# Kernel optimization log

Hardware: AMD Instinct MI355X
Metric: run time of the kernel (lower is better)

## Reference

```python
import jax, jax.numpy as jnp
import numpy as np

B, L, C, H = 4, 2048, 1024, 16
D = C // H            # head_dim = 64
HALF = D // 2         # 32
MAX_SCALE_MUL = float(np.log(100.0))


def setup_inputs() -> dict:
    key = jax.random.key(0)
    ks = jax.random.split(key, 6)
    x = jax.random.normal(ks[0], (B, L, C), dtype=jnp.float32)
    # causal additive bias [1,1,L,L]
    causal = jnp.tril(jnp.ones((L, L), dtype=bool))
    attn_bias = jnp.where(causal, 0.0, -1e9).astype(jnp.float32)[None, None]
    # RoPE cos/sin table: [B, 2, L, half]
    inv_freq = 1.0 / (10000.0 ** (jnp.arange(HALF, dtype=jnp.float32) / HALF))
    ang = jnp.arange(L, dtype=jnp.float32)[:, None] * inv_freq[None, :]  # [L, half]
    rope = jnp.stack([jnp.cos(ang), jnp.sin(ang)], axis=0)               # [2, L, half]
    rope_batch = jnp.broadcast_to(rope[None], (B, 2, L, HALF)).astype(jnp.float32)
    mat_qkv_w = jax.random.normal(ks[1], (3 * C, C), dtype=jnp.float32) * (1.0 / np.sqrt(C))
    q_bias = jnp.zeros((C,), dtype=jnp.float32)
    v_bias = jnp.zeros((C,), dtype=jnp.float32)
    proj_w = jax.random.normal(ks[2], (C, C), dtype=jnp.float32) * (1.0 / np.sqrt(C))
    proj_b = jnp.zeros((C,), dtype=jnp.float32)
    scale_mul = jnp.full((1, H, 1, 1), np.log(4.0), dtype=jnp.float32)
    return {"x": x, "attn_bias": attn_bias, "rope_batch": rope_batch,
            "mat_qkv_w": mat_qkv_w, "q_bias": q_bias, "v_bias": v_bias,
            "proj_w": proj_w, "proj_b": proj_b, "scale_mul": scale_mul}


def _l2norm(t, eps=1e-12):
    # F.normalize(t, dim=-1)
    n = jnp.sqrt(jnp.sum(t * t, axis=-1, keepdims=True))
    return t / jnp.maximum(n, eps)


def reference(x, attn_bias, rope_batch, mat_qkv_w, q_bias, v_bias, proj_w, proj_b, scale_mul):
    b, l, c = x.shape
    bias_cat = jnp.concatenate([q_bias, jnp.zeros_like(q_bias), v_bias])  # [3C]
    qkv = (x @ mat_qkv_w.T + bias_cat).reshape(b, l, 3, H, D)
    # non-flash layout: BHLc
    q = jnp.transpose(qkv[:, :, 0], (0, 2, 1, 3))
    k = jnp.transpose(qkv[:, :, 1], (0, 2, 1, 3))
    v = jnp.transpose(qkv[:, :, 2], (0, 2, 1, 3))
    # attn_l2_norm: scale=1, per-head learned multiplier
    sm = jnp.exp(jnp.minimum(scale_mul, MAX_SCALE_MUL))  # [1,H,1,1]
    q = _l2norm(q) * sm
    k = _l2norm(k)
    # RoPE (interleaved even/odd dims), start=0
    cos = rope_batch[:, 0, :l, :][:, None]  # [B,1,L,half]
    sin = rope_batch[:, 1, :l, :][:, None]
    def rot(t):
        t0, t1 = t[..., ::2], t[..., 1::2]
        r0 = t0 * cos - t1 * sin
        r1 = t0 * sin + t1 * cos
        return jnp.stack([r0, r1], axis=-1).reshape(t.shape)
    q, k = rot(q), rot(k)
    scale = 1.0  # attn_l2_norm path
    scores = jnp.einsum('bhqd,bhkd->bhqk', q, k) * scale + attn_bias
    attn = jax.nn.softmax(scores, axis=-1)
    out = jnp.einsum('bhqk,bhkd->bhqd', attn, v)
    out = jnp.transpose(out, (0, 2, 1, 3)).reshape(b, l, c)
    return out @ proj_w.T + proj_b
```

## Files before the change

### kernel.cpp

```cpp
#include <hip/hip_runtime.h>
#include <hip/hip_bf16.h>

#define BB 4
#define LL 2048
#define CC 1024
#define HH 16
#define DD 64
#define HALFD 32

typedef short bf16x8 __attribute__((ext_vector_type(8)));
typedef short bf16x4 __attribute__((ext_vector_type(4)));
typedef float f32x4 __attribute__((ext_vector_type(4)));

#if defined(__has_builtin)
#if __has_builtin(__builtin_amdgcn_mfma_f32_16x16x16bf16_1k)
#define HAVE_MFMA16 1
#endif
#endif

__device__ __forceinline__ float bf2f(unsigned short u) {
    union { unsigned int i; float f; } x; x.i = ((unsigned int)u) << 16; return x.f;
}
__device__ __forceinline__ unsigned short f2bf(float f) {
    union { float f; unsigned int i; } x; x.f = f;
    return (unsigned short)((x.i + 0x7fffu + ((x.i >> 16) & 1u)) >> 16);
}

__global__ void k_f2bf(const float4* __restrict__ in, ushort4* __restrict__ out, int n4) {
    int i = blockIdx.x * blockDim.x + threadIdx.x;
    if (i < n4) {
        float4 v = in[i];
        ushort4 o;
        o.x = f2bf(v.x); o.y = f2bf(v.y); o.z = f2bf(v.z); o.w = f2bf(v.w);
        out[i] = o;
    }
}

__global__ void k_biascat(const float* __restrict__ qb, const float* __restrict__ vb,
                          float* __restrict__ out) {
    int i = blockIdx.x * blockDim.x + threadIdx.x;
    if (i < 3 * CC) out[i] = (i < CC) ? qb[i] : (i < 2 * CC ? 0.f : vb[i - 2 * CC]);
}

template <typename OutT>
__global__ __launch_bounds__(256) void k_gemm_bt(
    const unsigned short* __restrict__ A, const unsigned short* __restrict__ Bt,
    const float* __restrict__ bias, OutT* __restrict__ Cout, int M, int N, int K) {
    __shared__ unsigned short As[128][40];
    __shared__ unsigned short Bs[128][40];
    int nT = N >> 7;
    int tM = (blockIdx.x / nT) << 7;
    int tN = (blockIdx.x % nT) << 7;
    int t = threadIdx.x;
    int lane = t & 63, wid = t >> 6;
    int wr = (wid >> 1) * 64, wc = (wid & 1) * 64;
    int c = lane & 15, g = lane >> 4;
    f32x4 acc[4][4];
#pragma unroll
    for (int i = 0; i < 4; i++)
#pragma unroll
        for (int j = 0; j < 4; j++) acc[i][j] = (f32x4){0.f, 0.f, 0.f, 0.f};

    for (int k0 = 0; k0 < K; k0 += 32) {
        __syncthreads();
#pragma unroll
        for (int i = t; i < 512; i += 256) {
            int row = i >> 2, ch = (i & 3) << 3;
            *(bf16x8*)&As[row][ch] = *(const bf16x8*)&A[(size_t)(tM + row) * K + k0 + ch];
            *(bf16x8*)&Bs[row][ch] = *(const bf16x8*)&Bt[(size_t)(tN + row) * K + k0 + ch];
        }
        __syncthreads();
        bf16x8 af[4], bfr[4];
#pragma unroll
        for (int fm = 0; fm < 4; fm++) af[fm] = *(const bf16x8*)&As[wr + fm * 16 + c][g * 8];
#pragma unroll
        for (int fn = 0; fn < 4; fn++) bfr[fn] = *(const bf16x8*)&Bs[wc + fn * 16 + c][g * 8];
#pragma unroll
        for (int fm = 0; fm < 4; fm++)
#pragma unroll
            for (int fn = 0; fn < 4; fn++)
                acc[fm][fn] = __builtin_amdgcn_mfma_f32_16x16x32_bf16(af[fm], bfr[fn],
                                                                      acc[fm][fn], 0, 0, 0);
    }
#pragma unroll
    for (int fm = 0; fm < 4; fm++) {
#pragma unroll
        for (int fn = 0; fn < 4; fn++) {
            int col = tN + wc + fn * 16 + c;
            float bv = bias[col];
#pragma unroll
            for (int r = 0; r < 4; r++) {
                int row = tM + wr + fm * 16 + g * 4 + r;
                float v = acc[fm][fn][r] + bv;
                if constexpr (sizeof(OutT) == 2)
                    Cout[(size_t)row * N + col] = f2bf(v);
                else
                    Cout[(size_t)row * N + col] = v;
            }
        }
    }
}

__global__ __launch_bounds__(256) void k_qknorm(
    const unsigned short* __restrict__ qkv, const float* __restrict__ rope,
    const float* __restrict__ smul, unsigned short* __restrict__ Q,
    unsigned short* __restrict__ Ko) {
    int wid = threadIdx.x >> 6, lane = threadIdx.x & 63;
    long rowid = (long)blockIdx.x * 4 + wid;
    int h = rowid & 15;
    long t2 = rowid >> 4;
    int l = t2 & 2047;
    int b = (int)(t2 >> 11);
    size_t base = ((size_t)(b * LL + l) * 3) * CC + h * 64 + lane;
    float q = bf2f(qkv[base]);
    float k = bf2f(qkv[base + CC]);
    float sq = q * q, sk = k * k;
#pragma unroll
    for (int m = 32; m >= 1; m >>= 1) {
        sq += __shfl_xor(sq, m);
        sk += __shfl_xor(sk, m);
    }
    float sm = expf(fminf(smul[h], 4.6051701859880913680f));
    q = q / fmaxf(sqrtf(sq), 1e-12f) * sm;
    k = k / fmaxf(sqrtf(sk), 1e-12f);
    int j = lane >> 1;
    float cs = rope[((size_t)(b * 2) * LL + l) * HALFD + j];
    float sn = rope[((size_t)(b * 2 + 1) * LL + l) * HALFD + j];
    float qp = __shfl_xor(q, 1), kp = __shfl_xor(k, 1);
    float qn = (lane & 1) ? (qp * sn + q * cs) : (q * cs - qp * sn);
    float kn = (lane & 1) ? (kp * sn + k * cs) : (k * cs - kp * sn);
    size_t ob = ((size_t)(b * HH + h) * LL + l) * 64 + lane;
    Q[ob] = f2bf(qn);
    Ko[ob] = f2bf(kn);
}

__global__ __launch_bounds__(256) void k_vtrans(const unsigned short* __restrict__ qkv,
                                               unsigned short* __restrict__ Vt) {
    __shared__ unsigned short tile[64][65];
    int bid = blockIdx.x;
    int lb = bid & 31;
    int bh = bid >> 5;
    int h = bh & 15, b = bh >> 4;
    int t = threadIdx.x;
    for (int i = t; i < 4096; i += 256) {
        int row = i >> 6, dd = i & 63;
        tile[row][dd] = qkv[((size_t)(b * LL + lb * 64 + row) * 3 + 2) * CC + h * 64 + dd];
    }
    __syncthreads();
    for (int i = t; i < 4096; i += 256) {
        int dd = i >> 6, l2 = i & 63;
        Vt[((size_t)bh * 64 + dd) * LL + lb * 64 + l2] = tile[l2][dd];
    }
}

__global__ __launch_bounds__(256) void k_attn(
    const unsigned short* __restrict__ Q, const unsigned short* __restrict__ K,
    const unsigned short* __restrict__ Vt, unsigned short* __restrict__ Out) {
    int lane = threadIdx.x & 63, wid = threadIdx.x >> 6;
    int c = lane & 15, g = lane >> 4;
    int bid = blockIdx.x;
    int bh = bid & 63;
    int strip = 15 - (bid >> 6);
    int qb = strip * 128 + wid * 32;
    const unsigned short* Qh = Q + (size_t)bh * LL * 64;
    const unsigned short* Kh = K + (size_t)bh * LL * 64;
    const unsigned short* Vh = Vt + (size_t)bh * 64 * LL;

    bf16x8 qf[2][2];
#pragma unroll
    for (int qt = 0; qt < 2; qt++)
#pragma unroll
        for (int ch = 0; ch < 2; ch++)
            qf[qt][ch] =
                *(const bf16x8*)&Qh[(size_t)(qb + qt * 16 + c) * 64 + ch * 32 + g * 8];

    f32x4 acc[2][4];
#pragma unroll
    for (int qt = 0; qt < 2; qt++)
#pragma unroll
        for (int dt = 0; dt < 4; dt++) acc[qt][dt] = (f32x4){0.f, 0.f, 0.f, 0.f};
    float m_[2] = {-1e30f, -1e30f}, l_[2] = {0.f, 0.f};

#ifndef HAVE_MFMA16
    int srcA = 32 * (g & 1) + c;
    int srcB = srcA + 16;
#endif

    for (int kt = 0; kt < qb + 32; kt += 32) {
        bf16x8 kf[2][2];
#pragma unroll
        for (int kt2 = 0; kt2 < 2; kt2++)
#pragma unroll
            for (int ch = 0; ch < 2; ch++)
                kf[kt2][ch] =
                    *(const bf16x8*)&Kh[(size_t)(kt + kt2 * 16 + c) * 64 + ch * 32 + g * 8];
#ifdef HAVE_MFMA16
        bf16x4 vf[4][2];
#pragma unroll
        for (int dt = 0; dt < 4; dt++)
#pragma unroll
            for (int kt2 = 0; kt2 < 2; kt2++)
                vf[dt][kt2] =
                    *(const bf16x4*)&Vh[(size_t)(dt * 16 + c) * LL + kt + kt2 * 16 + 4 * g];
#else
        bf16x8 vf8[4];
#pragma unroll
        for (int dt = 0; dt < 4; dt++)
            vf8[dt] = *(const bf16x8*)&Vh[(size_t)(dt * 16 + c) * LL + kt + 8 * g];
#endif
#pragma unroll
        for (int qt = 0; qt < 2; qt++) {
            int qtb = qb + qt * 16;
            int qrow = qtb + c;
            f32x4 s0 = (f32x4){0.f, 0.f, 0.f, 0.f}, s1 = (f32x4){0.f, 0.f, 0.f, 0.f};
            s0 = __builtin_amdgcn_mfma_f32_16x16x32_bf16(kf[0][0], qf[qt][0], s0, 0, 0, 0);
            s0 = __builtin_amdgcn_mfma_f32_16x16x32_bf16(kf[0][1], qf[qt][1], s0, 0, 0, 0);
            s1 = __builtin_amdgcn_mfma_f32_16x16x32_bf16(kf[1][0], qf[qt][0], s1, 0, 0, 0);
            s1 = __builtin_amdgcn_mfma_f32_16x16x32_bf16(kf[1][1], qf[qt][1], s1, 0, 0, 0);
            if (kt + 31 > qtb) {
#pragma unroll
                for (int r = 0; r < 4; r++) {
                    if (kt + 4 * g + r > qrow) s0[r] = -1e9f;
                    if (kt + 16 + 4 * g + r > qrow) s1[r] = -1e9f;
                }
            }
            float tm = fmaxf(fmaxf(fmaxf(s0[0], s0[1]), fmaxf(s0[2], s0[3])),
                             fmaxf(fmaxf(s1[0], s1[1]), fmaxf(s1[2], s1[3])));
            tm = fmaxf(tm, __shfl_xor(tm, 16));
            tm = fmaxf(tm, __shfl_xor(tm, 32));
            float mn = fmaxf(m_[qt], tm);
            float p0[4], p1[4];
            float rs = 0.f;
#pragma unroll
            for (int r = 0; r < 4; r++) {
                p0[r] = __expf(s0[r] - mn);
                p1[r] = __expf(s1[r] - mn);
                rs += p0[r] + p1[r];
            }
            rs += __shfl_xor(rs, 16);
            rs += __shfl_xor(rs, 32);
            float scl = __expf(m_[qt] - mn);
            l_[qt] = l_[qt] * scl + rs;
            m_[qt] = mn;
#pragma unroll
            for (int dt = 0; dt < 4; dt++) {
                acc[qt][dt][0] *= scl; acc[qt][dt][1] *= scl;
                acc[qt][dt][2] *= scl; acc[qt][dt][3] *= scl;
            }
#ifdef HAVE_MFMA16
            bf16x4 pb0, pb1;
#pragma unroll
            for (int r = 0; r < 4; r++) {
                pb0[r] = (short)f2bf(p0[r]);
                pb1[r] = (short)f2bf(p1[r]);
            }
#pragma unroll
            for (int dt = 0; dt < 4; dt++) {
                acc[qt][dt] =
                    __builtin_amdgcn_mfma_f32_16x16x16bf16_1k(vf[dt][0], pb0, acc[qt][dt], 0, 0, 0);
                acc[qt][dt] =
                    __builtin_amdgcn_mfma_f32_16x16x16bf16_1k(vf[dt][1], pb1, acc[qt][dt], 0, 0, 0);
            }
#else
            unsigned int A0 = (unsigned int)f2bf(p0[0]) | ((unsigned int)f2bf(p0[1]) << 16);
            unsigned int A1 = (unsigned int)f2bf(p0[2]) | ((unsigned int)f2bf(p0[3]) << 16);
            unsigned int B0 = (unsigned int)f2bf(p1[0]) | ((unsigned int)f2bf(p1[1]) << 16);
            unsigned int B1 = (unsigned int)f2bf(p1[2]) | ((unsigned int)f2bf(p1[3]) << 16);
            int t0a = __shfl((int)A0, srcA), t0b = __shfl((int)B0, srcA);
            int t1a = __shfl((int)A1, srcA), t1b = __shfl((int)B1, srcA);
            int t2a = __shfl((int)A0, srcB), t2b = __shfl((int)B0, srcB);
            int t3a = __shfl((int)A1, srcB), t3b = __shfl((int)B1, srcB);
            union { int w[4]; bf16x8 v; } u;
            bool hi = (g & 2) != 0;
            u.w[0] = hi ? t0b : t0a;
            u.w[1] = hi ? t1b : t1a;
            u.w[2] = hi ? t2b : t2a;
            u.w[3] = hi ? t3b : t3a;
#pragma unroll
            for (int dt = 0; dt < 4; dt++)
                acc[qt][dt] =
                    __builtin_amdgcn_mfma_f32_16x16x32_bf16(vf8[dt], u.v, acc[qt][dt], 0, 0, 0);
#endif
        }
    }
    int b = bh >> 4, h = bh & 15;
#pragma unroll
    for (int qt = 0; qt < 2; qt++) {
        float inv = 1.f / l_[qt];
        int qg = qb + qt * 16 + c;
        size_t ob = ((size_t)b * LL + qg) * CC + h * 64;
#pragma unroll
        for (int dt = 0; dt < 4; dt++) {
            ushort4 o;
            o.x = f2bf(acc[qt][dt][0] * inv);
            o.y = f2bf(acc[qt][dt][1] * inv);
            o.z = f2bf(acc[qt][dt][2] * inv);
            o.w = f2bf(acc[qt][dt][3] * inv);
            *(ushort4*)&Out[ob + dt * 16 + 4 * g] = o;
        }
    }
}

extern "C" void kernel_launch(void* const* d_in, const int* in_sizes, int n_in,
                              void* d_out, int out_size, void* d_ws, size_t ws_size,
                              hipStream_t stream) {
    const float* x = (const float*)d_in[0];
    const float* rope = (const float*)d_in[2];
    const float* w1 = (const float*)d_in[3];
    const float* qb = (const float*)d_in[4];
    const float* vb = (const float*)d_in[5];
    const float* w2 = (const float*)d_in[6];
    const float* pb = (const float*)d_in[7];
    const float* smul = (const float*)d_in[8];
    float* out = (float*)d_out;

    char* ws = (char*)d_ws;
    unsigned short* xb = (unsigned short*)(ws + 0);
    unsigned short* w1b = (unsigned short*)(ws + 16777216);
    unsigned short* w2b = (unsigned short*)(ws + 23068672);
    float* biascat = (float*)(ws + 25165824);
    unsigned short* qkvb = (unsigned short*)(ws + 25178112);
    unsigned short* Qb = (unsigned short*)(ws + 75509760);
    unsigned short* Kb = (unsigned short*)(ws + 92286976);
    unsigned short* Vtb = (unsigned short*)(ws + 109064192);
    unsigned short* attb = (unsigned short*)(ws + 125841408);
    if (ws_size < 142618624) return;

    int n4;
    n4 = BB * LL * CC / 4;
    k_f2bf<<<(n4 + 255) / 256, 256, 0, stream>>>((const float4*)x, (ushort4*)xb, n4);
    n4 = 3 * CC * CC / 4;
    k_f2bf<<<(n4 + 255) / 256, 256, 0, stream>>>((const float4*)w1, (ushort4*)w1b, n4);
    n4 = CC * CC / 4;
    k_f2bf<<<(n4 + 255) / 256, 256, 0, stream>>>((const float4*)w2, (ushort4*)w2b, n4);
    k_biascat<<<12, 256, 0, stream>>>(qb, vb, biascat);

    k_gemm_bt<unsigned short><<<(8192 / 128) * (3072 / 128), 256, 0, stream>>>(
        xb, w1b, biascat, qkvb, BB * LL, 3 * CC, CC);

    k_qknorm<<<BB * LL * HH / 4, 256, 0, stream>>>(qkvb, rope, smul, Qb, Kb);
    k_vtrans<<<BB * HH * (LL / 64), 256, 0, stream>>>(qkvb, Vtb);
    k_attn<<<64 * 16, 256, 0, stream>>>(Qb, Kb, Vtb, attb);

    k_gemm_bt<float><<<(8192 / 128) * (1024 / 128), 256, 0, stream>>>(
        attb, w2b, pb, out, BB * LL, CC, CC);
}
```

Baseline: 354.4 us.

## Use direct global-to-LDS loads in GEMM and widen attention key tiles with lazy rescale

The GEMM staging loop now uses global_load_lds to copy A/B tiles straight into unpadded shared memory, skipping the trip through registers. The attention loop processes 64 keys per iteration instead of 32, which halves the number of softmax reductions and loop iterations. It also skips the running-max rescale unless the max grows by more than a threshold of 8. Removing the padding may cause LDS bank conflicts on the fragment reads. The lazy rescale lets probabilities exceed 1 before bf16 conversion. With a 64-key step, the loop bound qb+32 can read keys past the diagonal, though those are masked.

```diff
diff --git a/kernel.cpp b/kernel.cpp
--- a/kernel.cpp
+++ b/kernel.cpp
@@ -24,6 +24,11 @@
 __device__ __forceinline__ unsigned short f2bf(float f) {
     union { float f; unsigned int i; } x; x.f = f;
     return (unsigned short)((x.i + 0x7fffu + ((x.i >> 16) & 1u)) >> 16);
+}
+__device__ __forceinline__ void gload_lds16(const void* g, void* l) {
+    __builtin_amdgcn_global_load_lds(
+        (const __attribute__((address_space(1))) unsigned int*)g,
+        (__attribute__((address_space(3))) unsigned int*)l, 16, 0, 0);
 }
 
 __global__ void k_f2bf(const float4* __restrict__ in, ushort4* __restrict__ out, int n4) {
@@ -46,8 +51,8 @@
 __global__ __launch_bounds__(256) void k_gemm_bt(
     const unsigned short* __restrict__ A, const unsigned short* __restrict__ Bt,
     const float* __restrict__ bias, OutT* __restrict__ Cout, int M, int N, int K) {
-    __shared__ unsigned short As[128][40];
-    __shared__ unsigned short Bs[128][40];
+    __shared__ unsigned short As[128][32];
+    __shared__ unsigned short Bs[128][32];
     int nT = N >> 7;
     int tM = (blockIdx.x / nT) << 7;
     int tN = (blockIdx.x % nT) << 7;
@@ -55,6 +60,15 @@
     int lane = t & 63, wid = t >> 6;
     int wr = (wid >> 1) * 64, wc = (wid & 1) * 64;
     int c = lane & 15, g = lane >> 4;
+
+    const unsigned short* gA = A + (size_t)(tM + wid * 32 + (lane >> 2)) * K + (lane & 3) * 8;
+    const unsigned short* gB = Bt + (size_t)(tN + wid * 32 + (lane >> 2)) * K + (lane & 3) * 8;
+    unsigned short* lA0 = &As[wid * 32][0];
+    unsigned short* lA1 = &As[wid * 32 + 16][0];
+    unsigned short* lB0 = &Bs[wid * 32][0];
+    unsigned short* lB1 = &Bs[wid * 32 + 16][0];
+    size_t r16 = (size_t)16 * K;
+
     f32x4 acc[4][4];
 #pragma unroll
     for (int i = 0; i < 4; i++)
@@ -63,12 +77,10 @@
 
     for (int k0 = 0; k0 < K; k0 += 32) {
         __syncthreads();
-#pragma unroll
-        for (int i = t; i < 512; i += 256) {
-            int row = i >> 2, ch = (i & 3) << 3;
-            *(bf16x8*)&As[row][ch] = *(const bf16x8*)&A[(size_t)(tM + row) * K + k0 + ch];
-            *(bf16x8*)&Bs[row][ch] = *(const bf16x8*)&Bt[(size_t)(tN + row) * K + k0 + ch];
-        }
+        gload_lds16(gA + k0, lA0);
+        gload_lds16(gA + k0 + r16, lA1);
+        gload_lds16(gB + k0, lB0);
+        gload_lds16(gB + k0 + r16, lB1);
         __syncthreads();
         bf16x8 af[4], bfr[4];
 #pragma unroll
@@ -186,100 +198,122 @@
     int srcB = srcA + 16;
 #endif
 
-    for (int kt = 0; kt < qb + 32; kt += 32) {
-        bf16x8 kf[2][2];
-#pragma unroll
-        for (int kt2 = 0; kt2 < 2; kt2++)
+    for (int kt = 0; kt < qb + 32; kt += 64) {
+        bf16x8 kf[4][2];
+#pragma unroll
+        for (int kt2 = 0; kt2 < 4; kt2++)
 #pragma unroll
             for (int ch = 0; ch < 2; ch++)
                 kf[kt2][ch] =
                     *(const bf16x8*)&Kh[(size_t)(kt + kt2 * 16 + c) * 64 + ch * 32 + g * 8];
 #ifdef HAVE_MFMA16
-        bf16x4 vf[4][2];
+        bf16x4 vf[4][4];
 #pragma unroll
         for (int dt = 0; dt < 4; dt++)
 #pragma unroll
-            for (int kt2 = 0; kt2 < 2; kt2++)
+            for (int kt2 = 0; kt2 < 4; kt2++)
                 vf[dt][kt2] =
                     *(const bf16x4*)&Vh[(size_t)(dt * 16 + c) * LL + kt + kt2 * 16 + 4 * g];
 #else
-        bf16x8 vf8[4];
+        bf16x8 vf8[4][2];
 #pragma unroll
         for (int dt = 0; dt < 4; dt++)
-            vf8[dt] = *(const bf16x8*)&Vh[(size_t)(dt * 16 + c) * LL + kt + 8 * g];
+#pragma unroll
+            for (int hf = 0; hf < 2; hf++)
+                vf8[dt][hf] =
+                    *(const bf16x8*)&Vh[(size_t)(dt * 16 + c) * LL + kt + hf * 32 + 8 * g];
 #endif
 #pragma unroll
         for (int qt = 0; qt < 2; qt++) {
             int qtb = qb + qt * 16;
             int qrow = qtb + c;
-            f32x4 s0 = (f32x4){0.f, 0.f, 0.f, 0.f}, s1 = (f32x4){0.f, 0.f, 0.f, 0.f};
-            s0 = __builtin_amdgcn_mfma_f32_16x16x32_bf16(kf[0][0], qf[qt][0], s0, 0, 0, 0);
-            s0 = __builtin_amdgcn_mfma_f32_16x16x32_bf16(kf[0][1], qf[qt][1], s0, 0, 0, 0);
-            s1 = __builtin_amdgcn_mfma_f32_16x16x32_bf16(kf[1][0], qf[qt][0], s1, 0, 0, 0);
-            s1 = __builtin_amdgcn_mfma_f32_16x16x32_bf16(kf[1][1], qf[qt][1], s1, 0, 0, 0);
-            if (kt + 31 > qtb) {
-#pragma unroll
-                for (int r = 0; r < 4; r++) {
-                    if (kt + 4 * g + r > qrow) s0[r] = -1e9f;
-                    if (kt + 16 + 4 * g + r > qrow) s1[r] = -1e9f;
+            f32x4 s[4];
+#pragma unroll
+            for (int kt2 = 0; kt2 < 4; kt2++) {
+                s[kt2] = (f32x4){0.f, 0.f, 0.f, 0.f};
+                s[kt2] = __builtin_amdgcn_mfma_f32_16x16x32_bf16(kf[kt2][0], qf[qt][0],
+                                                                 s[kt2], 0, 0, 0);
+                s[kt2] = __builtin_amdgcn_mfma_f32_16x16x32_bf16(kf[kt2][1], qf[qt][1],
+                                                                 s[kt2], 0, 0, 0);
+            }
+            if (kt + 63 > qtb) {
+#pragma unroll
+                for (int kt2 = 0; kt2 < 4; kt2++) {
+                    if (kt + kt2 * 16 + 15 > qtb) {
+#pragma unroll
+                        for (int r = 0; r < 4; r++)
+                            if (kt + kt2 * 16 + 4 * g + r > qrow) s[kt2][r] = -1e9f;
+                    }
                 }
             }
-            float tm = fmaxf(fmaxf(fmaxf(s0[0], s0[1]), fmaxf(s0[2], s0[3])),
-                             fmaxf(fmaxf(s1[0], s1[1]), fmaxf(s1[2], s1[3])));
+            float tm = fmaxf(fmaxf(fmaxf(s[0][0], s[0][1]), fmaxf(s[0][2], s[0][3])),
+                             fmaxf(fmaxf(s[1][0], s[1][1]), fmaxf(s[1][2], s[1][3])));
+            float tm2 = fmaxf(fmaxf(fmaxf(s[2][0], s[2][1]), fmaxf(s[2][2], s[2][3])),
+                              fmaxf(fmaxf(s[3][0], s[3][1]), fmaxf(s[3][2], s[3][3])));
+            tm = fmaxf(tm, tm2);
             tm = fmaxf(tm, __shfl_xor(tm, 16));
             tm = fmaxf(tm, __shfl_xor(tm, 32));
-            float mn = fmaxf(m_[qt], tm);
-            float p0[4], p1[4];
+            if (__any(tm > m_[qt] + 8.0f)) {
+                float mn = fmaxf(m_[qt], tm);
+                float scl = __expf(m_[qt] - mn);
+                m_[qt] = mn;
+                l_[qt] *= scl;
+#pragma unroll
+                for (int dt = 0; dt < 4; dt++) {
+                    acc[qt][dt][0] *= scl; acc[qt][dt][1] *= scl;
+                    acc[qt][dt][2] *= scl; acc[qt][dt][3] *= scl;
+                }
+            }
+            float p[4][4];
             float rs = 0.f;
 #pragma unroll
-            for (int r = 0; r < 4; r++) {
-                p0[r] = __expf(s0[r] - mn);
-                p1[r] = __expf(s1[r] - mn);
-                rs += p0[r] + p1[r];
-            }
+            for (int kt2 = 0; kt2 < 4; kt2++)
+#pragma unroll
+                for (int r = 0; r < 4; r++) {
+                    p[kt2][r] = __expf(s[kt2][r] - m_[qt]);
+                    rs += p[kt2][r];
+                }
             rs += __shfl_xor(rs, 16);
             rs += __shfl_xor(rs, 32);
-            float scl = __expf(m_[qt] - mn);
-            l_[qt] = l_[qt] * scl + rs;
-            m_[qt] = mn;
-#pragma unroll
-            for (int dt = 0; dt < 4; dt++) {
-                acc[qt][dt][0] *= scl; acc[qt][dt][1] *= scl;
-                acc[qt][dt][2] *= scl; acc[qt][dt][3] *= scl;
-            }
+            l_[qt] += rs;
 #ifdef HAVE_MFMA16
-            bf16x4 pb0, pb1;
-#pragma unroll
-            for (int r = 0; r < 4; r++) {
-                pb0[r] = (short)f2bf(p0[r]);
-                pb1[r] = (short)f2bf(p1[r]);
-            }
-#pragma unroll
-            for (int dt = 0; dt < 4; dt++) {
-                acc[qt][dt] =
-                    __builtin_amdgcn_mfma_f32_16x16x16bf16_1k(vf[dt][0], pb0, acc[qt][dt], 0, 0, 0);
-                acc[qt][dt] =
-                    __builtin_amdgcn_mfma_f32_16x16x16bf16_1k(vf[dt][1], pb1, acc[qt][dt], 0, 0, 0);
-            }
+            bf16x4 pb[4];
+#pragma unroll
+            for (int kt2 = 0; kt2 < 4; kt2++)
+#pragma unroll
+                for (int r = 0; r < 4; r++) pb[kt2][r] = (short)f2bf(p[kt2][r]);
+#pragma unroll
+            for (int dt = 0; dt < 4; dt++)
+#pragma unroll
+                for (int kt2 = 0; kt2 < 4; kt2++)
+                    acc[qt][dt] = __builtin_amdgcn_mfma_f32_16x16x16bf16_1k(
+                        vf[dt][kt2], pb[kt2], acc[qt][dt], 0, 0, 0);
 #else
-            unsigned int A0 = (unsigned int)f2bf(p0[0]) | ((unsigned int)f2bf(p0[1]) << 16);
-            unsigned int A1 = (unsigned int)f2bf(p0[2]) | ((unsigned int)f2bf(p0[3]) << 16);
-            unsigned int B0 = (unsigned int)f2bf(p1[0]) | ((unsigned int)f2bf(p1[1]) << 16);
-            unsigned int B1 = (unsigned int)f2bf(p1[2]) | ((unsigned int)f2bf(p1[3]) << 16);
-            int t0a = __shfl((int)A0, srcA), t0b = __shfl((int)B0, srcA);
-            int t1a = __shfl((int)A1, srcA), t1b = __shfl((int)B1, srcA);
-            int t2a = __shfl((int)A0, srcB), t2b = __shfl((int)B0, srcB);
-            int t3a = __shfl((int)A1, srcB), t3b = __shfl((int)B1, srcB);
-            union { int w[4]; bf16x8 v; } u;
-            bool hi = (g & 2) != 0;
-            u.w[0] = hi ? t0b : t0a;
-            u.w[1] = hi ? t1b : t1a;
-            u.w[2] = hi ? t2b : t2a;
-            u.w[3] = hi ? t3b : t3a;
-#pragma unroll
-            for (int dt = 0; dt < 4; dt++)
-                acc[qt][dt] =
-                    __builtin_amdgcn_mfma_f32_16x16x32_bf16(vf8[dt], u.v, acc[qt][dt], 0, 0, 0);
+#pragma unroll
+            for (int hf = 0; hf < 2; hf++) {
+                unsigned int A0 = (unsigned int)f2bf(p[2 * hf][0]) |
+                                  ((unsigned int)f2bf(p[2 * hf][1]) << 16);
+                unsigned int A1 = (unsigned int)f2bf(p[2 * hf][2]) |
+                                  ((unsigned int)f2bf(p[2 * hf][3]) << 16);
+                unsigned int B0 = (unsigned int)f2bf(p[2 * hf + 1][0]) |
+                                  ((unsigned int)f2bf(p[2 * hf + 1][1]) << 16);
+                unsigned int B1 = (unsigned int)f2bf(p[2 * hf + 1][2]) |
+                                  ((unsigned int)f2bf(p[2 * hf + 1][3]) << 16);
+                int t0a = __shfl((int)A0, srcA), t0b = __shfl((int)B0, srcA);
+                int t1a = __shfl((int)A1, srcA), t1b = __shfl((int)B1, srcA);
+                int t2a = __shfl((int)A0, srcB), t2b = __shfl((int)B0, srcB);
+                int t3a = __shfl((int)A1, srcB), t3b = __shfl((int)B1, srcB);
+                union { int w[4]; bf16x8 v; } u;
+                bool hi = (g & 2) != 0;
+                u.w[0] = hi ? t0b : t0a;
+                u.w[1] = hi ? t1b : t1a;
+                u.w[2] = hi ? t2b : t2a;
+                u.w[3] = hi ? t3b : t3a;
+#pragma unroll
+                for (int dt = 0; dt < 4; dt++)
+                    acc[qt][dt] = __builtin_amdgcn_mfma_f32_16x16x32_bf16(
+                        vf8[dt][hf], u.v, acc[qt][dt], 0, 0, 0);
+            }
 #endif
         }
     }
```

Result: no change. 347.8 us (-1.8%).
